# Performance work log

Hardware: AMD Instinct MI355X
Metric: run time of the kernel (lower is better)

Reference implementation:

```python
import jax, jax.numpy as jnp
import numpy as np

E, D, F = 32, 2048, 768  # num_experts, hidden_size, intermediate_size
B, S, TOPK = 2, 1024, 8
T = B * S


def setup_inputs() -> dict:
    key = jax.random.key(0)
    k1, k2, k3, k4, k5 = jax.random.split(key, 5)
    hidden_states = jax.random.normal(k1, (B, S, D), dtype=jnp.float32)
    routing_weights = jax.random.uniform(k2, (T, E), dtype=jnp.float32)
    router_indices = jax.random.randint(k3, (T, TOPK), 0, E)
    gate_up_proj = jax.random.normal(k4, (E, D, 2 * F), dtype=jnp.float32) * 0.02
    down_proj = jax.random.normal(k5, (E, F, D), dtype=jnp.float32) * 0.02
    return {
        "hidden_states": hidden_states,
        "routing_weights": routing_weights,
        "router_indices": router_indices,
        "gate_up_proj": gate_up_proj,
        "down_proj": down_proj,
    }


def reference(hidden_states, routing_weights, router_indices, gate_up_proj, down_proj):
    batch_size = hidden_states.shape[0]
    x = hidden_states.reshape(-1, D)  # (T, D)
    gate_up = jnp.einsum('TD,EDF->TEF', x, gate_up_proj)  # (T, E, 2F)
    gate, up = jnp.split(gate_up, 2, axis=-1)
    gated = up * jax.nn.silu(gate)  # (T, E, F)
    next_states = jnp.einsum('TEF,EFD->TED', gated, down_proj)  # (T, E, D)
    next_states = (next_states * routing_weights[..., None]).sum(axis=1)  # (T, D)
    return next_states.reshape(batch_size, -1, D)
```

## Files before the change

kernel.cpp:

```cpp
#include <hip/hip_runtime.h>
#include <stdint.h>

#define NE 32
#define ND 2048
#define NF 768
#define NF2 1536
#define NT 2048
#define NEF (NE * NF)
#define KH 12288

#define BM 128
#define BN 64
#define BK 32
#define BSTR 40

typedef __attribute__((ext_vector_type(8))) short short8;
typedef __attribute__((ext_vector_type(4))) float floatx4;

__device__ __forceinline__ unsigned pk_bf16(float a, float b) {
  union { float f; unsigned u; } ua, ub;
  ua.f = a; ub.f = b;
  unsigned ra = (ua.u + 0x7fffu + ((ua.u >> 16) & 1u)) >> 16;
  unsigned rb = (ub.u + 0x7fffu + ((ub.u >> 16) & 1u)) & 0xffff0000u;
  return ra | rb;
}
__device__ __forceinline__ unsigned short bf16_1(float a) {
  union { float f; unsigned u; } ua; ua.f = a;
  return (unsigned short)((ua.u + 0x7fffu + ((ua.u >> 16) & 1u)) >> 16);
}

#define GLOAD_LDS16(g, l)                                                     \
  __builtin_amdgcn_global_load_lds(                                           \
      (const __attribute__((address_space(1))) void*)(g),                     \
      (__attribute__((address_space(3))) void*)(l), 16, 0, 0)

__global__ void k_cvt_x(const float* __restrict__ x, unsigned short* __restrict__ xb, int n4) {
  int i = blockIdx.x * blockDim.x + threadIdx.x;
  if (i < n4) {
    float4 v = ((const float4*)x)[i];
    uint2 o;
    o.x = pk_bf16(v.x, v.y);
    o.y = pk_bf16(v.z, v.w);
    ((uint2*)xb)[i] = o;
  }
}

__global__ void k_trans(const float* __restrict__ in, unsigned short* __restrict__ out,
                        int R, int C, size_t zstride) {
  __shared__ float sT[64][65];
  in  += (size_t)blockIdx.z * zstride;
  out += (size_t)blockIdx.z * zstride;
  const int r0 = blockIdx.y * 64, c0 = blockIdx.x * 64;
  const int t = threadIdx.x;
  const int lrow = t >> 4, lc4 = (t & 15) * 4;
#pragma unroll
  for (int i = 0; i < 4; i++) {
    float4 v = *(const float4*)&in[(size_t)(r0 + lrow + i * 16) * C + c0 + lc4];
    sT[lrow + i * 16][lc4 + 0] = v.x;
    sT[lrow + i * 16][lc4 + 1] = v.y;
    sT[lrow + i * 16][lc4 + 2] = v.z;
    sT[lrow + i * 16][lc4 + 3] = v.w;
  }
  __syncthreads();
  const int c = t >> 2, rg = (t & 3) * 16;
  uint4 o0, o1;
  o0.x = pk_bf16(sT[rg + 0][c],  sT[rg + 1][c]);
  o0.y = pk_bf16(sT[rg + 2][c],  sT[rg + 3][c]);
  o0.z = pk_bf16(sT[rg + 4][c],  sT[rg + 5][c]);
  o0.w = pk_bf16(sT[rg + 6][c],  sT[rg + 7][c]);
  o1.x = pk_bf16(sT[rg + 8][c],  sT[rg + 9][c]);
  o1.y = pk_bf16(sT[rg + 10][c], sT[rg + 11][c]);
  o1.z = pk_bf16(sT[rg + 12][c], sT[rg + 13][c]);
  o1.w = pk_bf16(sT[rg + 14][c], sT[rg + 15][c]);
  unsigned short* op = &out[(size_t)(c0 + c) * R + r0 + rg];
  ((uint4*)op)[0] = o0;
  ((uint4*)op)[1] = o1;
}

__global__ __launch_bounds__(256, 3) void k_gemm1b(
    const unsigned short* __restrict__ xb,
    const unsigned short* __restrict__ w1t,
    const float* __restrict__ rw,
    unsigned short* __restrict__ gws,
    int e0)
{
  __shared__ unsigned short sA[BM * BK];
  __shared__ unsigned short sG[BN * BK];
  __shared__ unsigned short sU[BN * BK];
  __shared__ float srw[BM];

  const int el  = blockIdx.y;
  const int e   = e0 + el;
  const int mt  = blockIdx.x & 15;
  const int nt  = blockIdx.x >> 4;
  const int m0  = mt * BM, n0 = nt * BN;
  const int tid = threadIdx.x;
  const int wid = tid >> 6, lane = tid & 63;
  const int wm = wid >> 1, wn = wid & 1;
  const int l15 = lane & 15, q = lane >> 4;

  if (tid < BM) srw[tid] = rw[(size_t)(m0 + tid) * NE + e];

  floatx4 accG[4][2], accU[4][2];
#pragma unroll
  for (int i = 0; i < 4; i++)
#pragma unroll
    for (int j = 0; j < 2; j++) {
      accG[i][j] = (floatx4){0.f, 0.f, 0.f, 0.f};
      accU[i][j] = (floatx4){0.f, 0.f, 0.f, 0.f};
    }

  const unsigned short* w1e = w1t + (size_t)el * NF2 * ND;

  const int koff = (lane & 3) * 8;
  const unsigned short* aptr = xb + (size_t)(m0 + wid * 32 + (lane >> 2)) * ND + koff;
  unsigned short* aLds = &sA[wid * 32 * BK];
  const unsigned short* gptr = w1e + (size_t)(n0 + wid * 16 + (lane >> 2)) * ND + koff;
  const unsigned short* uptr = gptr + (size_t)NF * ND;
  unsigned short* gLds = &sG[wid * 16 * BK];
  unsigned short* uLds = &sU[wid * 16 * BK];

  for (int kb = 0; kb < ND / BK; ++kb) {
    __syncthreads();
    GLOAD_LDS16(aptr + kb * BK, aLds);
    GLOAD_LDS16(aptr + kb * BK + 16 * ND, aLds + 16 * BK);
    GLOAD_LDS16(gptr + kb * BK, gLds);
    GLOAD_LDS16(uptr + kb * BK, uLds);
    __syncthreads();

    short8 bg0 = *(const short8*)&sG[(wn * 32 + 0  + l15) * BK + q * 8];
    short8 bg1 = *(const short8*)&sG[(wn * 32 + 16 + l15) * BK + q * 8];
    short8 bu0 = *(const short8*)&sU[(wn * 32 + 0  + l15) * BK + q * 8];
    short8 bu1 = *(const short8*)&sU[(wn * 32 + 16 + l15) * BK + q * 8];
#pragma unroll
    for (int i = 0; i < 4; i++) {
      short8 af = *(const short8*)&sA[(wm * 64 + i * 16 + l15) * BK + q * 8];
      accG[i][0] = __builtin_amdgcn_mfma_f32_16x16x32_bf16(af, bg0, accG[i][0], 0, 0, 0);
      accG[i][1] = __builtin_amdgcn_mfma_f32_16x16x32_bf16(af, bg1, accG[i][1], 0, 0, 0);
      accU[i][0] = __builtin_amdgcn_mfma_f32_16x16x32_bf16(af, bu0, accU[i][0], 0, 0, 0);
      accU[i][1] = __builtin_amdgcn_mfma_f32_16x16x32_bf16(af, bu1, accU[i][1], 0, 0, 0);
    }
  }

  const size_t obase = (size_t)m0 * NEF + (size_t)e * NF + n0 + wn * 32;
#pragma unroll
  for (int i = 0; i < 4; i++)
#pragma unroll
    for (int j = 0; j < 2; j++)
#pragma unroll
      for (int r = 0; r < 4; r++) {
        int row = wm * 64 + i * 16 + q * 4 + r;
        float g = accG[i][j][r];
        float u = accU[i][j][r];
        float sig = __builtin_amdgcn_rcpf(1.f + __expf(-g));
        float val = u * g * sig * srw[row];
        gws[obase + (size_t)row * NEF + j * 16 + l15] = bf16_1(val);
      }
}

template<int KSTRIDE, int HITERS>
__global__ __launch_bounds__(256, 3) void k_gemm2b(
    const unsigned short* __restrict__ gb,
    const unsigned short* __restrict__ w2t,
    float* __restrict__ out,
    int kbase)
{
  __shared__ unsigned short sA[BM * BK];
  __shared__ unsigned short sB[BN * BK];

  const int mt = blockIdx.x & 15;
  const int nt = blockIdx.x >> 4;
  const int m0 = mt * BM, n0 = nt * BN;
  const int tid = threadIdx.x;
  const int wid = tid >> 6, lane = tid & 63;
  const int wm = wid >> 1, wn = wid & 1;
  const int l15 = lane & 15, q = lane >> 4;

  const int kb0 = blockIdx.y * HITERS;
  const int kb1 = kb0 + HITERS;

  floatx4 acc[4][2];
#pragma unroll
  for (int i = 0; i < 4; i++)
#pragma unroll
    for (int j = 0; j < 2; j++) acc[i][j] = (floatx4){0.f, 0.f, 0.f, 0.f};

  const int koff = (lane & 3) * 8;
  const unsigned short* aptr = gb + (size_t)(m0 + wid * 32 + (lane >> 2)) * NEF + kbase + koff;
  unsigned short* aLds = &sA[wid * 32 * BK];
  const unsigned short* bptr = w2t + (size_t)(n0 + wid * 16 + (lane >> 2)) * KSTRIDE + koff;
  unsigned short* bLds = &sB[wid * 16 * BK];

  for (int kb = kb0; kb < kb1; ++kb) {
    __syncthreads();
    GLOAD_LDS16(aptr + kb * BK, aLds);
    GLOAD_LDS16(aptr + kb * BK + 16 * NEF, aLds + 16 * BK);
    GLOAD_LDS16(bptr + kb * BK, bLds);
    __syncthreads();

    short8 b0 = *(const short8*)&sB[(wn * 32 + 0  + l15) * BK + q * 8];
    short8 b1 = *(const short8*)&sB[(wn * 32 + 16 + l15) * BK + q * 8];
#pragma unroll
    for (int i = 0; i < 4; i++) {
      short8 af = *(const short8*)&sA[(wm * 64 + i * 16 + l15) * BK + q * 8];
      acc[i][0] = __builtin_amdgcn_mfma_f32_16x16x32_bf16(af, b0, acc[i][0], 0, 0, 0);
      acc[i][1] = __builtin_amdgcn_mfma_f32_16x16x32_bf16(af, b1, acc[i][1], 0, 0, 0);
    }
  }

#pragma unroll
  for (int i = 0; i < 4; i++)
#pragma unroll
    for (int j = 0; j < 2; j++)
#pragma unroll
      for (int r = 0; r < 4; r++) {
        int row = wm * 64 + i * 16 + q * 4 + r;
        unsafeAtomicAdd(&out[(size_t)(m0 + row) * ND + n0 + wn * 32 + j * 16 + l15],
                        acc[i][j][r]);
      }
}

__global__ __launch_bounds__(256, 2) void k_gemm1_legacy(
    const unsigned short* __restrict__ xb, const float* __restrict__ w1,
    const float* __restrict__ rw, unsigned short* __restrict__ gws)
{
  __shared__ unsigned short sA[BM * BK];
  __shared__ unsigned short sG[BN * BSTR];
  __shared__ unsigned short sU[BN * BSTR];
  __shared__ float srw[BM];
  const int e = blockIdx.y, mt = blockIdx.x & 15, nt = blockIdx.x >> 4;
  const int m0 = mt * BM, n0 = nt * BN;
  const int tid = threadIdx.x, wid = tid >> 6, lane = tid & 63;
  const int wm = wid >> 1, wn = wid & 1, l15 = lane & 15, q = lane >> 4;
  if (tid < BM) srw[tid] = rw[(size_t)(m0 + tid) * NE + e];
  const float* w1e = w1 + (size_t)e * ND * (2 * NF);
  floatx4 accG[4][2], accU[4][2];
#pragma unroll
  for (int i = 0; i < 4; i++)
#pragma unroll
    for (int j = 0; j < 2; j++) {
      accG[i][j] = (floatx4){0.f, 0.f, 0.f, 0.f};
      accU[i][j] = (floatx4){0.f, 0.f, 0.f, 0.f};
    }
  const int arow = wid * 32 + (lane >> 2), akoff = (lane & 3) * 8;
  const unsigned short* aptr = xb + (size_t)(m0 + arow) * ND + akoff;
  unsigned short* aLds = &sA[wid * 32 * BK];
  const float* gptr0 = w1e + (size_t)(wid * 8) * (2 * NF) + n0 + lane;
  for (int kb = 0; kb < ND / BK; ++kb) {
    const float* gp = gptr0 + (size_t)kb * BK * (2 * NF);
    float gv[8], uv[8];
#pragma unroll
    for (int r = 0; r < 8; r++) {
      gv[r] = gp[(size_t)r * (2 * NF)];
      uv[r] = gp[(size_t)r * (2 * NF) + NF];
    }
    __syncthreads();
    GLOAD_LDS16(aptr + kb * BK, aLds);
    GLOAD_LDS16(aptr + kb * BK + 16 * ND, aLds + 16 * BK);
    uint4 wg, wu;
    wg.x = pk_bf16(gv[0], gv[1]); wg.y = pk_bf16(gv[2], gv[3]);
    wg.z = pk_bf16(gv[4], gv[5]); wg.w = pk_bf16(gv[6], gv[7]);
    wu.x = pk_bf16(uv[0], uv[1]); wu.y = pk_bf16(uv[2], uv[3]);
    wu.z = pk_bf16(uv[4], uv[5]); wu.w = pk_bf16(uv[6], uv[7]);
    *((uint4*)&sG[lane * BSTR + wid * 8]) = wg;
    *((uint4*)&sU[lane * BSTR + wid * 8]) = wu;
    __syncthreads();
    short8 bg0 = *(const short8*)&sG[(wn * 32 + 0  + l15) * BSTR + q * 8];
    short8 bg1 = *(const short8*)&sG[(wn * 32 + 16 + l15) * BSTR + q * 8];
    short8 bu0 = *(const short8*)&sU[(wn * 32 + 0  + l15) * BSTR + q * 8];
    short8 bu1 = *(const short8*)&sU[(wn * 32 + 16 + l15) * BSTR + q * 8];
#pragma unroll
    for (int i = 0; i < 4; i++) {
      short8 af = *(const short8*)&sA[(wm * 64 + i * 16 + l15) * BK + q * 8];
      accG[i][0] = __builtin_amdgcn_mfma_f32_16x16x32_bf16(af, bg0, accG[i][0], 0, 0, 0);
      accG[i][1] = __builtin_amdgcn_mfma_f32_16x16x32_bf16(af, bg1, accG[i][1], 0, 0, 0);
      accU[i][0] = __builtin_amdgcn_mfma_f32_16x16x32_bf16(af, bu0, accU[i][0], 0, 0, 0);
      accU[i][1] = __builtin_amdgcn_mfma_f32_16x16x32_bf16(af, bu1, accU[i][1], 0, 0, 0);
    }
  }
  const size_t obase = (size_t)m0 * NEF + (size_t)e * NF + n0 + wn * 32;
#pragma unroll
  for (int i = 0; i < 4; i++)
#pragma unroll
    for (int j = 0; j < 2; j++)
#pragma unroll
      for (int r = 0; r < 4; r++) {
        int row = wm * 64 + i * 16 + q * 4 + r;
        float g = accG[i][j][r], u = accU[i][j][r];
        float sig = __builtin_amdgcn_rcpf(1.f + __expf(-g));
        gws[obase + (size_t)row * NEF + j * 16 + l15] = bf16_1(u * g * sig * srw[row]);
      }
}

__global__ __launch_bounds__(256, 2) void k_gemm2_legacy(
    const unsigned short* __restrict__ gb, const float* __restrict__ w2,
    float* __restrict__ out)
{
  __shared__ unsigned short sA[BM * BK];
  __shared__ unsigned short sB[BN * BSTR];
  const int mt = blockIdx.x & 15, nt = blockIdx.x >> 4;
  const int m0 = mt * BM, n0 = nt * BN;
  const int tid = threadIdx.x, wid = tid >> 6, lane = tid & 63;
  const int wm = wid >> 1, wn = wid & 1, l15 = lane & 15, q = lane >> 4;
  const int kb0 = blockIdx.y * (NEF / BK / 4), kb1 = kb0 + (NEF / BK / 4);
  floatx4 acc[4][2];
#pragma unroll
  for (int i = 0; i < 4; i++)
#pragma unroll
    for (int j = 0; j < 2; j++) acc[i][j] = (floatx4){0.f, 0.f, 0.f, 0.f};
  const int arow = wid * 32 + (lane >> 2), akoff = (lane & 3) * 8;
  const unsigned short* aptr = gb + (size_t)(m0 + arow) * NEF + akoff;
  unsigned short* aLds = &sA[wid * 32 * BK];
  const float* bptr0 = w2 + (size_t)(wid * 8) * ND + n0 + lane;
  for (int kb = kb0; kb < kb1; ++kb) {
    const float* bp = bptr0 + (size_t)kb * BK * ND;
    float bv[8];
#pragma unroll
    for (int r = 0; r < 8; r++) bv[r] = bp[(size_t)r * ND];
    __syncthreads();
    GLOAD_LDS16(aptr + kb * BK, aLds);
    GLOAD_LDS16(aptr + kb * BK + 16 * NEF, aLds + 16 * BK);
    uint4 wb;
    wb.x = pk_bf16(bv[0], bv[1]); wb.y = pk_bf16(bv[2], bv[3]);
    wb.z = pk_bf16(bv[4], bv[5]); wb.w = pk_bf16(bv[6], bv[7]);
    *((uint4*)&sB[lane * BSTR + wid * 8]) = wb;
    __syncthreads();
    short8 b0 = *(const short8*)&sB[(wn * 32 + 0  + l15) * BSTR + q * 8];
    short8 b1 = *(const short8*)&sB[(wn * 32 + 16 + l15) * BSTR + q * 8];
#pragma unroll
    for (int i = 0; i < 4; i++) {
      short8 af = *(const short8*)&sA[(wm * 64 + i * 16 + l15) * BK + q * 8];
      acc[i][0] = __builtin_amdgcn_mfma_f32_16x16x32_bf16(af, b0, acc[i][0], 0, 0, 0);
      acc[i][1] = __builtin_amdgcn_mfma_f32_16x16x32_bf16(af, b1, acc[i][1], 0, 0, 0);
    }
  }
#pragma unroll
  for (int i = 0; i < 4; i++)
#pragma unroll
    for (int j = 0; j < 2; j++)
#pragma unroll
      for (int r = 0; r < 4; r++) {
        int row = wm * 64 + i * 16 + q * 4 + r;
        unsafeAtomicAdd(&out[(size_t)(m0 + row) * ND + n0 + wn * 32 + j * 16 + l15],
                        acc[i][j][r]);
      }
}

extern "C" void kernel_launch(void* const* d_in, const int* in_sizes, int n_in,
                              void* d_out, int out_size, void* d_ws, size_t ws_size,
                              hipStream_t stream) {
  const float* x  = (const float*)d_in[0];
  const float* rw = (const float*)d_in[1];
  const float* w1 = (const float*)d_in[3];
  const float* w2 = (const float*)d_in[4];
  float* out = (float*)d_out;

  unsigned short* xb  = (unsigned short*)d_ws;
  unsigned short* gb  = xb + (size_t)NT * ND;
  unsigned short* wtb = gb + (size_t)NT * NEF;
  unsigned short* w1t = wtb;
  unsigned short* w2t = w1t + (size_t)NE * NF2 * ND;
  const size_t WS_FULL = ((size_t)NT * ND + (size_t)NT * NEF +
                          (size_t)NE * NF2 * ND + (size_t)ND * NEF) * 2;
  const size_t WS_NEED = ((size_t)NT * ND + (size_t)NT * NEF +
                          (size_t)8 * NF2 * ND) * 2;

  hipMemsetAsync(out, 0, (size_t)out_size * sizeof(float), stream);
  k_cvt_x<<<(NT * ND / 4 + 255) / 256, 256, 0, stream>>>(x, xb, NT * ND / 4);

  if (ws_size >= WS_FULL) {
    {
      dim3 gt(NF2 / 64, ND / 64, NE);
      k_trans<<<gt, 256, 0, stream>>>(w1, w1t, ND, NF2, (size_t)ND * NF2);
    }
    {
      dim3 gt(ND / 64, NEF / 64, 1);
      k_trans<<<gt, 256, 0, stream>>>(w2, w2t, NEF, ND, 0);
    }
    {
      dim3 g1(16 * (NF / BN), NE);
      k_gemm1b<<<g1, 256, 0, stream>>>(xb, w1t, rw, gb, 0);
    }
    {
      dim3 g2(16 * (ND / BN), 2);
      k_gemm2b<NEF, NEF / BK / 2><<<g2, 256, 0, stream>>>(gb, w2t, out, 0);
    }
  } else if (ws_size >= WS_NEED) {
    for (int qc = 0; qc < 4; ++qc) {
      dim3 gt(NF2 / 64, ND / 64, 8);
      k_trans<<<gt, 256, 0, stream>>>(w1 + (size_t)qc * 8 * ND * NF2, wtb,
                                      ND, NF2, (size_t)ND * NF2);
      dim3 g1(16 * (NF / BN), 8);
      k_gemm1b<<<g1, 256, 0, stream>>>(xb, wtb, rw, gb, qc * 8);
    }
    for (int h = 0; h < 2; ++h) {
      dim3 gt(ND / 64, KH / 64, 1);
      k_trans<<<gt, 256, 0, stream>>>(w2 + (size_t)h * KH * ND, wtb, KH, ND, 0);
      dim3 g2(16 * (ND / BN), 2);
      k_gemm2b<KH, KH / BK / 2><<<g2, 256, 0, stream>>>(gb, wtb, out, h * KH);
    }
  } else {
    dim3 gA(16 * (NF / BN), NE);
    k_gemm1_legacy<<<gA, 256, 0, stream>>>(xb, w1, rw, gb);
    dim3 gB(16 * (ND / BN), 4);
    k_gemm2_legacy<<<gB, 256, 0, stream>>>(gb, w2, out);
  }
}
```

Baseline: 1.503 ms.

## Add 256x256 pipelined gate/up GEMM with interleaved weight layout

Replaces the first GEMM on the full-workspace path with a new 512-thread kernel that computes 256x256 output tiles over 64-wide K steps. It double-buffers LDS through direct global-to-LDS loads, uses an XOR-swizzled layout and priority hints around the MFMA bursts, and remaps block indices so that consecutive blocks are spread across experts. The weight transpose now interleaves gate and up columns in 32-wide groups, so one tile holds matching gate and up columns and the SiLU product is fused in the epilogue. The intent is to raise MFMA utilisation and data reuse compared with the old 128x64 tiles, at the cost of heavy hand scheduling with inline waitcnt and barriers, higher register pressure and lower occupancy.

Measured after the change: 1.426 ms. 5.1% less time.

```diff
diff --git a/kernel.cpp b/kernel.cpp
--- a/kernel.cpp
+++ b/kernel.cpp
@@ -33,6 +33,8 @@
   __builtin_amdgcn_global_load_lds(                                           \
       (const __attribute__((address_space(1))) void*)(g),                     \
       (__attribute__((address_space(3))) void*)(l), 16, 0, 0)
+
+#define MF(a, b, c) __builtin_amdgcn_mfma_f32_16x16x32_bf16(a, b, c, 0, 0, 0)
 
 __global__ void k_cvt_x(const float* __restrict__ x, unsigned short* __restrict__ xb, int n4) {
   int i = blockIdx.x * blockDim.x + threadIdx.x;
@@ -45,6 +47,7 @@
   }
 }
 
+template <int PAIR>
 __global__ void k_trans(const float* __restrict__ in, unsigned short* __restrict__ out,
                         int R, int C, size_t zstride) {
   __shared__ float sT[64][65];
@@ -72,9 +75,159 @@
   o1.y = pk_bf16(sT[rg + 10][c], sT[rg + 11][c]);
   o1.z = pk_bf16(sT[rg + 12][c], sT[rg + 13][c]);
   o1.w = pk_bf16(sT[rg + 14][c], sT[rg + 15][c]);
-  unsigned short* op = &out[(size_t)(c0 + c) * R + r0 + rg];
+  int oc = c0 + c;
+  if (PAIR) {
+    oc = (oc < NF) ? (((oc >> 5) << 6) + (oc & 31))
+                   : ((((oc - NF) >> 5) << 6) + 32 + ((oc - NF) & 31));
+  }
+  unsigned short* op = &out[(size_t)oc * R + r0 + rg];
   ((uint4*)op)[0] = o0;
   ((uint4*)op)[1] = o1;
+}
+
+__global__ __launch_bounds__(512, 2) void k_gemm1p(
+    const unsigned short* __restrict__ xb,
+    const unsigned short* __restrict__ w1t,
+    const float* __restrict__ rw,
+    unsigned short* __restrict__ gws)
+{
+  __shared__ unsigned short sA[2][2][8192];
+  __shared__ unsigned short sB[2][2][8192];
+  __shared__ float srw[256];
+
+  const int bx = blockIdx.x;
+  const int L  = (bx & 7) * 192 + (bx >> 3);
+  const int e  = L / 48;
+  const int rem = L - e * 48;
+  const int mt = rem & 7, nt = rem >> 3;
+  const int m0 = mt * 256, n0 = nt * 256;
+
+  const int tid = threadIdx.x;
+  const int wid = tid >> 6, lane = tid & 63;
+  const int wm2 = wid >> 2, wn4 = wid & 3;
+  const int l15 = lane & 15, qg = lane >> 4;
+  const int hb = wn4 >> 1, rbB = (wn4 & 1) * 64;
+
+  if (tid < 256) srw[tid] = rw[(size_t)(m0 + tid) * NE + e];
+
+  const int aoff0 = l15 * 64 + ((qg * 8) ^ ((l15 & 7) << 3));
+  const int aoff1 = l15 * 64 + (((32 + qg * 8)) ^ ((l15 & 7) << 3));
+
+  const int r8 = tid >> 3;
+  const int csrc = ((tid & 7) ^ (r8 & 7)) * 8;
+  const unsigned short* w1e = w1t + (size_t)e * NF2 * ND;
+  const unsigned short* aSrc = xb  + (size_t)(m0 + r8) * ND + csrc;
+  const unsigned short* bSrc = w1e + (size_t)(n0 + r8) * ND + csrc;
+
+#define STAGE_A(buf, h, kt) do {                                              \
+    const unsigned short* _g = aSrc + (size_t)(h) * 128 * ND + (size_t)(kt) * 64; \
+    GLOAD_LDS16(_g, &sA[buf][h][wid * 512]);                                  \
+    GLOAD_LDS16(_g + (size_t)64 * ND, &sA[buf][h][wid * 512 + 4096]);         \
+  } while (0)
+#define STAGE_B(buf, h, kt) do {                                              \
+    const unsigned short* _g = bSrc + (size_t)(h) * 128 * ND + (size_t)(kt) * 64; \
+    GLOAD_LDS16(_g, &sB[buf][h][wid * 512]);                                  \
+    GLOAD_LDS16(_g + (size_t)64 * ND, &sB[buf][h][wid * 512 + 4096]);         \
+  } while (0)
+
+#define DS_A(buf, q) {                                                        \
+    a0s0 = *(const short8*)&sA[buf][wm2][((q) * 32 +  0) * 64 + aoff0];       \
+    a0s1 = *(const short8*)&sA[buf][wm2][((q) * 32 +  0) * 64 + aoff1];       \
+    a1s0 = *(const short8*)&sA[buf][wm2][((q) * 32 + 16) * 64 + aoff0];       \
+    a1s1 = *(const short8*)&sA[buf][wm2][((q) * 32 + 16) * 64 + aoff1];       \
+  }
+#define DS_B(buf) {                                                           \
+    b0s0 = *(const short8*)&sB[buf][hb][(rbB +  0) * 64 + aoff0];             \
+    b0s1 = *(const short8*)&sB[buf][hb][(rbB +  0) * 64 + aoff1];             \
+    b1s0 = *(const short8*)&sB[buf][hb][(rbB + 16) * 64 + aoff0];             \
+    b1s1 = *(const short8*)&sB[buf][hb][(rbB + 16) * 64 + aoff1];             \
+    b2s0 = *(const short8*)&sB[buf][hb][(rbB + 32) * 64 + aoff0];             \
+    b2s1 = *(const short8*)&sB[buf][hb][(rbB + 32) * 64 + aoff1];             \
+    b3s0 = *(const short8*)&sB[buf][hb][(rbB + 48) * 64 + aoff0];             \
+    b3s1 = *(const short8*)&sB[buf][hb][(rbB + 48) * 64 + aoff1];             \
+  }
+#define MM(q) do {                                                            \
+    __builtin_amdgcn_s_setprio(1);                                            \
+    acc[(q)*2+0][0] = MF(a0s0, b0s0, acc[(q)*2+0][0]);                        \
+    acc[(q)*2+0][0] = MF(a0s1, b0s1, acc[(q)*2+0][0]);                        \
+    acc[(q)*2+0][1] = MF(a0s0, b1s0, acc[(q)*2+0][1]);                        \
+    acc[(q)*2+0][1] = MF(a0s1, b1s1, acc[(q)*2+0][1]);                        \
+    acc[(q)*2+0][2] = MF(a0s0, b2s0, acc[(q)*2+0][2]);                        \
+    acc[(q)*2+0][2] = MF(a0s1, b2s1, acc[(q)*2+0][2]);                        \
+    acc[(q)*2+0][3] = MF(a0s0, b3s0, acc[(q)*2+0][3]);                        \
+    acc[(q)*2+0][3] = MF(a0s1, b3s1, acc[(q)*2+0][3]);                        \
+    acc[(q)*2+1][0] = MF(a1s0, b0s0, acc[(q)*2+1][0]);                        \
+    acc[(q)*2+1][0] = MF(a1s1, b0s1, acc[(q)*2+1][0]);                        \
+    acc[(q)*2+1][1] = MF(a1s0, b1s0, acc[(q)*2+1][1]);                        \
+    acc[(q)*2+1][1] = MF(a1s1, b1s1, acc[(q)*2+1][1]);                        \
+    acc[(q)*2+1][2] = MF(a1s0, b2s0, acc[(q)*2+1][2]);                        \
+    acc[(q)*2+1][2] = MF(a1s1, b2s1, acc[(q)*2+1][2]);                        \
+    acc[(q)*2+1][3] = MF(a1s0, b3s0, acc[(q)*2+1][3]);                        \
+    acc[(q)*2+1][3] = MF(a1s1, b3s1, acc[(q)*2+1][3]);                        \
+    __builtin_amdgcn_s_setprio(0);                                            \
+  } while (0)
+
+#define BAR_OPEN  asm volatile("s_barrier" ::: "memory")
+#define BAR_CLOSE asm volatile("s_waitcnt lgkmcnt(0)\n\ts_barrier" ::: "memory")
+#define VM4 asm volatile("s_waitcnt vmcnt(4)" ::: "memory")
+#define VM0 asm volatile("s_waitcnt vmcnt(0)" ::: "memory")
+#define S23_ON(x) x
+#define S23_OFF(x)
+
+#define KITER(t1, t2, t3, S23, VMT)                                           \
+  DS_A(0, 0) DS_B(0) STAGE_A(1, 0, t1); BAR_OPEN; MM(0); BAR_CLOSE;           \
+  DS_A(0, 1) STAGE_A(1, 1, t1); BAR_OPEN; MM(1); BAR_CLOSE;                   \
+  DS_A(0, 2) S23(STAGE_B(0, 0, t2);) BAR_OPEN; MM(2); BAR_CLOSE;              \
+  DS_A(0, 3) S23(STAGE_B(0, 1, t2);) VMT; BAR_OPEN; MM(3); BAR_CLOSE;         \
+  DS_A(1, 0) DS_B(1) S23(STAGE_A(0, 0, t2);) BAR_OPEN; MM(0); BAR_CLOSE;      \
+  DS_A(1, 1) S23(STAGE_A(0, 1, t2);) BAR_OPEN; MM(1); BAR_CLOSE;              \
+  DS_A(1, 2) S23(STAGE_B(1, 0, t3);) BAR_OPEN; MM(2); BAR_CLOSE;              \
+  DS_A(1, 3) S23(STAGE_B(1, 1, t3);) VMT; BAR_OPEN; MM(3); BAR_CLOSE;
+
+  short8 a0s0, a0s1, a1s0, a1s1;
+  short8 b0s0, b0s1, b1s0, b1s1, b2s0, b2s1, b3s0, b3s1;
+  floatx4 acc[8][4];
+#pragma unroll
+  for (int i = 0; i < 8; i++)
+#pragma unroll
+    for (int j = 0; j < 4; j++) acc[i][j] = (floatx4){0.f, 0.f, 0.f, 0.f};
+
+  STAGE_B(0, 0, 0); STAGE_B(0, 1, 0);
+  STAGE_A(0, 0, 0); STAGE_A(0, 1, 0);
+  STAGE_B(1, 0, 1); STAGE_B(1, 1, 1);
+  VM4; BAR_OPEN;
+
+  const int nI = ND / 64 / 2;
+  for (int i = 0; i < nI - 1; ++i) {
+    const int t1 = 2 * i + 1, t2 = 2 * i + 2, t3 = 2 * i + 3;
+    KITER(t1, t2, t3, S23_ON, VM4)
+  }
+  {
+    const int t1 = ND / 64 - 1;
+    KITER(t1, 0, 0, S23_OFF, VM0)
+  }
+
+  const size_t cb = (size_t)e * NF + (size_t)nt * 128 + wn4 * 32 + l15;
+#pragma unroll
+  for (int mf = 0; mf < 8; ++mf) {
+    const int rbase = wm2 * 128 + mf * 16 + qg * 4;
+#pragma unroll
+    for (int nf = 0; nf < 2; ++nf)
+#pragma unroll
+      for (int r = 0; r < 4; ++r) {
+        float g = acc[mf][nf][r];
+        float u = acc[mf][nf + 2][r];
+        float sig = __builtin_amdgcn_rcpf(1.f + __expf(-g));
+        float val = u * g * sig * srw[rbase + r];
+        gws[(size_t)(m0 + rbase + r) * NEF + cb + nf * 16] = bf16_1(val);
+      }
+  }
+#undef STAGE_A
+#undef STAGE_B
+#undef DS_A
+#undef DS_B
+#undef MM
+#undef KITER
 }
 
 __global__ __launch_bounds__(256, 3) void k_gemm1b(
@@ -135,10 +288,10 @@
 #pragma unroll
     for (int i = 0; i < 4; i++) {
       short8 af = *(const short8*)&sA[(wm * 64 + i * 16 + l15) * BK + q * 8];
-      accG[i][0] = __builtin_amdgcn_mfma_f32_16x16x32_bf16(af, bg0, accG[i][0], 0, 0, 0);
-      accG[i][1] = __builtin_amdgcn_mfma_f32_16x16x32_bf16(af, bg1, accG[i][1], 0, 0, 0);
-      accU[i][0] = __builtin_amdgcn_mfma_f32_16x16x32_bf16(af, bu0, accU[i][0], 0, 0, 0);
-      accU[i][1] = __builtin_amdgcn_mfma_f32_16x16x32_bf16(af, bu1, accU[i][1], 0, 0, 0);
+      accG[i][0] = MF(af, bg0, accG[i][0]);
+      accG[i][1] = MF(af, bg1, accG[i][1]);
+      accU[i][0] = MF(af, bu0, accU[i][0]);
+      accU[i][1] = MF(af, bu1, accU[i][1]);
     }
   }
 
@@ -203,8 +356,8 @@
 #pragma unroll
     for (int i = 0; i < 4; i++) {
       short8 af = *(const short8*)&sA[(wm * 64 + i * 16 + l15) * BK + q * 8];
-      acc[i][0] = __builtin_amdgcn_mfma_f32_16x16x32_bf16(af, b0, acc[i][0], 0, 0, 0);
-      acc[i][1] = __builtin_amdgcn_mfma_f32_16x16x32_bf16(af, b1, acc[i][1], 0, 0, 0);
+      acc[i][0] = MF(af, b0, acc[i][0]);
+      acc[i][1] = MF(af, b1, acc[i][1]);
     }
   }
 
@@ -272,10 +425,10 @@
 #pragma unroll
     for (int i = 0; i < 4; i++) {
       short8 af = *(const short8*)&sA[(wm * 64 + i * 16 + l15) * BK + q * 8];
-      accG[i][0] = __builtin_amdgcn_mfma_f32_16x16x32_bf16(af, bg0, accG[i][0], 0, 0, 0);
-      accG[i][1] = __builtin_amdgcn_mfma_f32_16x16x32_bf16(af, bg1, accG[i][1], 0, 0, 0);
-      accU[i][0] = __builtin_amdgcn_mfma_f32_16x16x32_bf16(af, bu0, accU[i][0], 0, 0, 0);
-      accU[i][1] = __builtin_amdgcn_mfma_f32_16x16x32_bf16(af, bu1, accU[i][1], 0, 0, 0);
+      accG[i][0] = MF(af, bg0, accG[i][0]);
+      accG[i][1] = MF(af, bg1, accG[i][1]);
+      accU[i][0] = MF(af, bu0, accU[i][0]);
+      accU[i][1] = MF(af, bu1, accU[i][1]);
     }
   }
   const size_t obase = (size_t)m0 * NEF + (size_t)e * NF + n0 + wn * 32;
@@ -330,8 +483,8 @@
 #pragma unroll
     for (int i = 0; i < 4; i++) {
       short8 af = *(const short8*)&sA[(wm * 64 + i * 16 + l15) * BK + q * 8];
-      acc[i][0] = __builtin_amdgcn_mfma_f32_16x16x32_bf16(af, b0, acc[i][0], 0, 0, 0);
-      acc[i][1] = __builtin_amdgcn_mfma_f32_16x16x32_bf16(af, b1, acc[i][1], 0, 0, 0);
+      acc[i][0] = MF(af, b0, acc[i][0]);
+      acc[i][1] = MF(af, b1, acc[i][1]);
     }
   }
 #pragma unroll
@@ -371,16 +524,13 @@
   if (ws_size >= WS_FULL) {
     {
       dim3 gt(NF2 / 64, ND / 64, NE);
-      k_trans<<<gt, 256, 0, stream>>>(w1, w1t, ND, NF2, (size_t)ND * NF2);
+      k_trans<1><<<gt, 256, 0, stream>>>(w1, w1t, ND, NF2, (size_t)ND * NF2);
     }
     {
       dim3 gt(ND / 64, NEF / 64, 1);
-      k_trans<<<gt, 256, 0, stream>>>(w2, w2t, NEF, ND, 0);
-    }
-    {
-      dim3 g1(16 * (NF / BN), NE);
-      k_gemm1b<<<g1, 256, 0, stream>>>(xb, w1t, rw, gb, 0);
-    }
+      k_trans<0><<<gt, 256, 0, stream>>>(w2, w2t, NEF, ND, 0);
+    }
+    k_gemm1p<<<dim3(8 * 6 * NE), 512, 0, stream>>>(xb, w1t, rw, gb);
     {
       dim3 g2(16 * (ND / BN), 2);
       k_gemm2b<NEF, NEF / BK / 2><<<g2, 256, 0, stream>>>(gb, w2t, out, 0);
@@ -388,14 +538,14 @@
   } else if (ws_size >= WS_NEED) {
     for (int qc = 0; qc < 4; ++qc) {
       dim3 gt(NF2 / 64, ND / 64, 8);
-      k_trans<<<gt, 256, 0, stream>>>(w1 + (size_t)qc * 8 * ND * NF2, wtb,
-                                      ND, NF2, (size_t)ND * NF2);
+      k_trans<0><<<gt, 256, 0, stream>>>(w1 + (size_t)qc * 8 * ND * NF2, wtb,
+                                         ND, NF2, (size_t)ND * NF2);
       dim3 g1(16 * (NF / BN), 8);
       k_gemm1b<<<g1, 256, 0, stream>>>(xb, wtb, rw, gb, qc * 8);
     }
     for (int h = 0; h < 2; ++h) {
       dim3 gt(ND / 64, KH / 64, 1);
-      k_trans<<<gt, 256, 0, stream>>>(w2 + (size_t)h * KH * ND, wtb, KH, ND, 0);
+      k_trans<0><<<gt, 256, 0, stream>>>(w2 + (size_t)h * KH * ND, wtb, KH, ND, 0);
       dim3 g2(16 * (ND / BN), 2);
       k_gemm2b<KH, KH / BK / 2><<<g2, 256, 0, stream>>>(gb, wtb, out, h * KH);
     }
```
